# Performance work log

Hardware: AMD Instinct MI355X
Metric: run time of the kernel (lower is better)

Reference implementation:

```python
import jax, jax.numpy as jnp
import numpy as np
from jax import lax

B, T, LM, H = 16, 60, 63, 64   # batch, frames, landmark dim, lstm hidden
IMG_H, IMG_W = 240, 320
CONV_FEAT = 252                 # 4 * 7 * 9


def _conv(x, w, b, s):
    # x: [N, Cin, H, W], w: [Cout, Cin, kh, kw], VALID padding, stride s
    y = lax.conv_general_dilated(x, w, (s, s), 'VALID',
                                 dimension_numbers=('NCHW', 'OIHW', 'NCHW'))
    return y + b[None, :, None, None]


def setup_inputs() -> dict:
    key = jax.random.key(0)
    ks = jax.random.split(key, 24)
    s = 0.05
    d = {
        'input': jax.random.normal(ks[0], (B, T, LM), jnp.float32),
        'video': jax.random.uniform(ks[1], (B, T, IMG_H, IMG_W), jnp.float32),
        'W00': jax.random.normal(ks[2], (LM, LM), jnp.float32) * s,
        'b00': jnp.zeros((LM,), jnp.float32),
        'W01': jax.random.normal(ks[3], (64, LM), jnp.float32) * s,
        'b01': jnp.zeros((64,), jnp.float32),
        'Wc0': jax.random.normal(ks[4], (16, 1, 5, 5), jnp.float32) * s,
        'bc0': jnp.zeros((16,), jnp.float32),
        'Wc1': jax.random.normal(ks[5], (16, 16, 5, 5), jnp.float32) * s,
        'bc1': jnp.zeros((16,), jnp.float32),
        'Wc2': jax.random.normal(ks[6], (4, 16, 2, 2), jnp.float32) * s,
        'bc2': jnp.zeros((4,), jnp.float32),
        'Wih': jax.random.normal(ks[7], (4 * H, 64 + CONV_FEAT), jnp.float32) * s,
        'Whh': jax.random.normal(ks[8], (4 * H, H), jnp.float32) * s,
        'bih': jnp.zeros((4 * H,), jnp.float32),
        'bhh': jnp.zeros((4 * H,), jnp.float32),
        'W10': jax.random.normal(ks[9], (32, H), jnp.float32) * s,
        'b10': jnp.zeros((32,), jnp.float32),
        'W11': jax.random.normal(ks[10], (32, 32), jnp.float32) * s,
        'b11': jnp.zeros((32,), jnp.float32),
        'W12': jax.random.normal(ks[11], (256, 32), jnp.float32) * s,
        'b12': jnp.zeros((256,), jnp.float32),
    }
    return d


def reference(input, video, W00, b00, W01, b01, Wc0, bc0, Wc1, bc1, Wc2, bc2,
              Wih, Whh, bih, bhh, W10, b10, W11, b11, W12, b12):
    relu = jax.nn.relu
    # per-frame landmark MLP, vectorized over all frames: [B, T, 64]
    f = relu(jnp.einsum('btl,ml->btm', input, W00) + b00)
    f = relu(jnp.einsum('btl,ml->btm', f, W01) + b01)
    # per-frame conv features, all frames in one batched conv: [B*T, 1, 240, 320]
    v = video.reshape(B * T, 1, IMG_H, IMG_W)
    v = relu(_conv(v, Wc0, bc0, 4))          # [B*T, 16, 59, 79]
    v = relu(_conv(v, Wc1, bc1, 4))          # [B*T, 16, 14, 19]
    v = relu(_conv(v, Wc2, bc2, 2))          # [B*T, 4, 7, 9]
    v = v.reshape(B, T, CONV_FEAT)
    # frame inputs to LSTM: [B, T, 316]
    x = jnp.concatenate([f, v], axis=-1)
    # Torch semantics: LSTM called unbatched with 2D input [B, 316] per frame,
    # so the batch dim is consumed as a sequence; state carries across frames.
    # Total sequence is frame-major: [T, B, 316] -> [T*B, 316].
    seq = x.transpose(1, 0, 2).reshape(T * B, -1)

    def step(carry, xt):
        h, c = carry
        g = xt @ Wih.T + bih + h @ Whh.T + bhh
        i, fg, gg, o = jnp.split(g, 4)
        c = jax.nn.sigmoid(fg) * c + jax.nn.sigmoid(i) * jnp.tanh(gg)
        h = jax.nn.sigmoid(o) * jnp.tanh(c)
        return (h, c), h

    h0 = jnp.zeros((H,), seq.dtype)
    _, hs = lax.scan(step, (h0, h0), seq)    # [T*B, H]
    out = hs[-B:]                            # last frame's full output: [B, H]
    out = relu(out @ W10.T + b10)
    out = relu(out @ W11.T + b11)
    return out @ W12.T + b12                 # [B, 256]
```

## Files before the change

kernel.cpp:

```cpp
#include <hip/hip_runtime.h>
#include <math.h>

#define B_   16
#define T_   60
#define LMD  63
#define IH   240
#define IW   320
#define XDIM 316
#define NSEQ 960

#define X_BYTES   1213440
#define G_BYTES   983040

__device__ __forceinline__ float rl(float v, int k) {
    return __uint_as_float((unsigned)__builtin_amdgcn_readlane((int)__float_as_uint(v), k));
}
__device__ __forceinline__ float sig_f(float x) {
    return __builtin_amdgcn_rcpf(1.0f + __expf(-x));
}
__device__ __forceinline__ float tanh_f(float x) {
    return 1.0f - 2.0f * __builtin_amdgcn_rcpf(__expf(2.0f * x) + 1.0f);
}

__global__ void k_mlp(const float* __restrict__ inp,
                      const float* __restrict__ W00, const float* __restrict__ b00,
                      const float* __restrict__ W01, const float* __restrict__ b01,
                      float* __restrict__ X) {
    __shared__ float x0s[LMD], f1s[LMD];
    int bt = blockIdx.x;
    int b = bt / T_, t = bt % T_;
    int s = t * B_ + b;
    int m = threadIdx.x;
    if (m < LMD) x0s[m] = inp[bt * LMD + m];
    __syncthreads();
    if (m < LMD) {
        const float* wr = W00 + m * LMD;
        float a0 = 0.f, a1 = 0.f, a2 = 0.f, a3 = 0.f;
        for (int k = 0; k < 60; k += 4) {
            a0 += x0s[k + 0] * wr[k + 0];
            a1 += x0s[k + 1] * wr[k + 1];
            a2 += x0s[k + 2] * wr[k + 2];
            a3 += x0s[k + 3] * wr[k + 3];
        }
        a0 += x0s[60] * wr[60]; a1 += x0s[61] * wr[61]; a2 += x0s[62] * wr[62];
        f1s[m] = fmaxf(((a0 + a1) + (a2 + a3)) + b00[m], 0.f);
    }
    __syncthreads();
    {
        const float* wr = W01 + m * LMD;
        float a0 = 0.f, a1 = 0.f, a2 = 0.f, a3 = 0.f;
        for (int k = 0; k < 60; k += 4) {
            a0 += f1s[k + 0] * wr[k + 0];
            a1 += f1s[k + 1] * wr[k + 1];
            a2 += f1s[k + 2] * wr[k + 2];
            a3 += f1s[k + 3] * wr[k + 3];
        }
        a0 += f1s[60] * wr[60]; a1 += f1s[61] * wr[61]; a2 += f1s[62] * wr[62];
        X[(size_t)s * XDIM + m] = fmaxf(((a0 + a1) + (a2 + a3)) + b01[m], 0.f);
    }
}

__global__ __launch_bounds__(256, 1) void k_conv(const float* __restrict__ video,
        const float* __restrict__ Wc0, const float* __restrict__ bc0,
        const float* __restrict__ Wc1, const float* __restrict__ bc1,
        const float* __restrict__ Wc2, const float* __restrict__ bc2,
        float* __restrict__ X) {
    __shared__ float W0T[26 * 16];
    __shared__ float band[16 * 408];
    __shared__ float part[19 * 4 * 17];
    __shared__ float c1L[14 * 19 * 17];
    int tid = threadIdx.x;
    int bt = blockIdx.x;
    int b = bt / T_, t = bt % T_;
    int s = t * B_ + b;
    const float* vid = video + (size_t)bt * (IH * IW);

    int ch1 = tid & 15, ic = tid >> 4;
    int wave = tid >> 6, lane = tid & 63;

    int d0 = tid / 79, c0c0 = tid % 79;
    int pos1 = tid + 256;
    bool has1 = (pos1 < 395);
    int d1 = has1 ? pos1 / 79 : 0, c0c1 = has1 ? pos1 % 79 : 0;

    for (int i = tid; i < 400; i += 256) { int ch = i / 25, tap = i % 25; W0T[tap * 16 + ch] = Wc0[i]; }
    if (tid < 16) W0T[25 * 16 + tid] = bc0[tid];
    float w1r[25];
#pragma unroll
    for (int tap = 0; tap < 25; ++tap)
        w1r[tap] = Wc1[(ch1 * 16 + ic) * 25 + tap];

    float PX0[25], PX1[25];
    {
        const float* vb = vid + (4 * d0) * IW + c0c0 * 4;
#pragma unroll
        for (int kr = 0; kr < 5; ++kr) {
            float4 v = *(const float4*)(vb + kr * IW);
            PX0[kr*5+0]=v.x; PX0[kr*5+1]=v.y; PX0[kr*5+2]=v.z; PX0[kr*5+3]=v.w;
            PX0[kr*5+4]=vb[kr*IW+4];
        }
        if (has1) {
            const float* vc = vid + (4 * d1) * IW + c0c1 * 4;
#pragma unroll
            for (int kr = 0; kr < 5; ++kr) {
                float4 v = *(const float4*)(vc + kr * IW);
                PX1[kr*5+0]=v.x; PX1[kr*5+1]=v.y; PX1[kr*5+2]=v.z; PX1[kr*5+3]=v.w;
                PX1[kr*5+4]=vc[kr*IW+4];
            }
        }
    }
    __syncthreads();

    for (int r1 = 0; r1 < 14; ++r1) {
        {
            float acc[16];
            {
                const float4* b4 = (const float4*)&W0T[25 * 16];
                float4 ba = b4[0], bb = b4[1], bc = b4[2], bd = b4[3];
                acc[0]=ba.x; acc[1]=ba.y; acc[2]=ba.z; acc[3]=ba.w;
                acc[4]=bb.x; acc[5]=bb.y; acc[6]=bb.z; acc[7]=bb.w;
                acc[8]=bc.x; acc[9]=bc.y; acc[10]=bc.z; acc[11]=bc.w;
                acc[12]=bd.x; acc[13]=bd.y; acc[14]=bd.z; acc[15]=bd.w;
            }
#pragma unroll
            for (int tap = 0; tap < 25; ++tap) {
                float p = PX0[tap];
                const float4* w4 = (const float4*)&W0T[tap * 16];
                float4 wa = w4[0], wb = w4[1], wc = w4[2], wd = w4[3];
                acc[0]+=p*wa.x; acc[1]+=p*wa.y; acc[2]+=p*wa.z; acc[3]+=p*wa.w;
                acc[4]+=p*wb.x; acc[5]+=p*wb.y; acc[6]+=p*wb.z; acc[7]+=p*wb.w;
                acc[8]+=p*wc.x; acc[9]+=p*wc.y; acc[10]+=p*wc.z; acc[11]+=p*wc.w;
                acc[12]+=p*wd.x; acc[13]+=p*wd.y; acc[14]+=p*wd.z; acc[15]+=p*wd.w;
            }
#pragma unroll
            for (int ch = 0; ch < 16; ++ch)
                band[ch * 408 + d0 * 80 + c0c0] = fmaxf(acc[ch], 0.f);
        }
        if (has1) {
            float acc[16];
            {
                const float4* b4 = (const float4*)&W0T[25 * 16];
                float4 ba = b4[0], bb = b4[1], bc = b4[2], bd = b4[3];
                acc[0]=ba.x; acc[1]=ba.y; acc[2]=ba.z; acc[3]=ba.w;
                acc[4]=bb.x; acc[5]=bb.y; acc[6]=bb.z; acc[7]=bb.w;
                acc[8]=bc.x; acc[9]=bc.y; acc[10]=bc.z; acc[11]=bc.w;
                acc[12]=bd.x; acc[13]=bd.y; acc[14]=bd.z; acc[15]=bd.w;
            }
#pragma unroll
            for (int tap = 0; tap < 25; ++tap) {
                float p = PX1[tap];
                const float4* w4 = (const float4*)&W0T[tap * 16];
                float4 wa = w4[0], wb = w4[1], wc = w4[2], wd = w4[3];
                acc[0]+=p*wa.x; acc[1]+=p*wa.y; acc[2]+=p*wa.z; acc[3]+=p*wa.w;
                acc[4]+=p*wb.x; acc[5]+=p*wb.y; acc[6]+=p*wb.z; acc[7]+=p*wb.w;
                acc[8]+=p*wc.x; acc[9]+=p*wc.y; acc[10]+=p*wc.z; acc[11]+=p*wc.w;
                acc[12]+=p*wd.x; acc[13]+=p*wd.y; acc[14]+=p*wd.z; acc[15]+=p*wd.w;
            }
#pragma unroll
            for (int ch = 0; ch < 16; ++ch)
                band[ch * 408 + d1 * 80 + c0c1] = fmaxf(acc[ch], 0.f);
        }

        if (r1 + 1 < 14) {
            const float* vb = vid + (16 * (r1+1) + 4 * d0) * IW + c0c0 * 4;
#pragma unroll
            for (int kr = 0; kr < 5; ++kr) {
                float4 v = *(const float4*)(vb + kr * IW);
                PX0[kr*5+0]=v.x; PX0[kr*5+1]=v.y; PX0[kr*5+2]=v.z; PX0[kr*5+3]=v.w;
                PX0[kr*5+4]=vb[kr*IW+4];
            }
            if (has1) {
                const float* vc = vid + (16 * (r1+1) + 4 * d1) * IW + c0c1 * 4;
#pragma unroll
                for (int kr = 0; kr < 5; ++kr) {
                    float4 v = *(const float4*)(vc + kr * IW);
                    PX1[kr*5+0]=v.x; PX1[kr*5+1]=v.y; PX1[kr*5+2]=v.z; PX1[kr*5+3]=v.w;
                    PX1[kr*5+4]=vc[kr*IW+4];
                }
            }
        }
        __syncthreads();

        const float* bb0 = &band[ic * 408];
        for (int c1c = 0; c1c < 19; ++c1c) {
            const float* bb = bb0 + c1c * 4;
            float a0, a1, a2, a3, a4;
            {
                float4 v = *(const float4*)(bb);       float sc = bb[4];
                a0 = v.x*w1r[0]  + v.y*w1r[1]  + v.z*w1r[2]  + v.w*w1r[3]  + sc*w1r[4];
            }
            {
                float4 v = *(const float4*)(bb + 80);  float sc = bb[84];
                a1 = v.x*w1r[5]  + v.y*w1r[6]  + v.z*w1r[7]  + v.w*w1r[8]  + sc*w1r[9];
            }
            {
                float4 v = *(const float4*)(bb + 160); float sc = bb[164];
                a2 = v.x*w1r[10] + v.y*w1r[11] + v.z*w1r[12] + v.w*w1r[13] + sc*w1r[14];
            }
            {
                float4 v = *(const float4*)(bb + 240); float sc = bb[244];
                a3 = v.x*w1r[15] + v.y*w1r[16] + v.z*w1r[17] + v.w*w1r[18] + sc*w1r[19];
            }
            {
                float4 v = *(const float4*)(bb + 320); float sc = bb[324];
                a4 = v.x*w1r[20] + v.y*w1r[21] + v.z*w1r[22] + v.w*w1r[23] + sc*w1r[24];
            }
            float p = ((a0 + a1) + (a2 + a3)) + a4;
            p += __shfl_xor(p, 16);
            p += __shfl_xor(p, 32);
            if (lane < 16)
                part[c1c * 68 + wave * 17 + ch1] = p;
        }
        __syncthreads();

        for (int o = tid; o < 304; o += 256) {
            int c1c = o >> 4, ch = o & 15;
            const float* pp = &part[c1c * 68 + ch];
            float v = bc1[ch] + pp[0] + pp[17] + pp[34] + pp[51];
            c1L[(r1 * 19 + c1c) * 17 + ch] = fmaxf(v, 0.f);
        }
        __syncthreads();
    }

    for (int o = tid; o < 252; o += 256) {
        int ch2 = o / 63, rr = (o / 9) % 7, cc = o % 9;
        float a = bc2[ch2];
        for (int ic2 = 0; ic2 < 16; ++ic2)
            for (int kr = 0; kr < 2; ++kr)
                for (int kc = 0; kc < 2; ++kc)
                    a += c1L[((2 * rr + kr) * 19 + 2 * cc + kc) * 17 + ic2] *
                         Wc2[((ch2 * 16 + ic2) * 2 + kr) * 2 + kc];
        X[(size_t)s * XDIM + 64 + o] = fmaxf(a, 0.f);
    }
}

__global__ void k_gpre(const float* __restrict__ X, const float* __restrict__ Wih,
                       const float* __restrict__ bih, const float* __restrict__ bhh,
                       float* __restrict__ G) {
    int s = blockIdx.x;
    int j = threadIdx.x;
    const float4* x4 = (const float4*)(X + (size_t)s * XDIM);
    const float4* w4 = (const float4*)(Wih + (size_t)j * XDIM);
    float a0 = 0.f, a1 = 0.f, a2 = 0.f, a3 = 0.f;
    for (int ko = 0; ko < 79; ++ko) {
        float4 w = w4[ko], x = x4[ko];
        a0 += w.x * x.x;
        a1 += w.y * x.y;
        a2 += w.z * x.z;
        a3 += w.w * x.w;
    }
    G[(size_t)s * 256 + j] = ((a0 + a1) + (a2 + a3)) + (bih[j] + bhh[j]);
}

#define REPW(M) M(0) M(1) M(2) M(3) M(4) M(5) M(6) M(7) \
                M(8) M(9) M(10) M(11) M(12) M(13) M(14) M(15)

__global__ __launch_bounds__(256, 1) void k_scan(const float* __restrict__ G,
        const float* __restrict__ Whh,
        const float* __restrict__ W10, const float* __restrict__ b10,
        const float* __restrict__ W11, const float* __restrict__ b11,
        const float* __restrict__ W12, const float* __restrict__ b12,
        float* __restrict__ out) {
    __shared__ float act[2][256];
    __shared__ float hsL[16 * 64];
    __shared__ float m1s[32], m2s[32];
    int j = threadIdx.x;
    int w = j >> 6, l = j & 63;

#define DECLW(n) float4 wv##n;
    REPW(DECLW)
#undef DECLW
    {
        const float4* Wr = (const float4*)(Whh + (size_t)j * 64);
#define LOADW(n) wv##n = Wr[n];
        REPW(LOADW)
#undef LOADW
    }

    float h = 0.f, c = 0.f;
    float gcur = G[j];

    for (int t = 0; t < NSEQ; ++t) {
        float gnext = (t + 1 < NSEQ) ? G[(size_t)(t + 1) * 256 + j] : 0.f;

        float a0 = gcur, a1 = 0.f, a2 = 0.f, a3 = 0.f;
#define GFMA(n) { \
        float h0 = rl(h, 4*(n)+0), h1 = rl(h, 4*(n)+1); \
        float h2 = rl(h, 4*(n)+2), h3 = rl(h, 4*(n)+3); \
        a0 += h0 * wv##n.x; a1 += h1 * wv##n.y; \
        a2 += h2 * wv##n.z; a3 += h3 * wv##n.w; \
    }
        REPW(GFMA)
#undef GFMA
        float g = (a0 + a1) + (a2 + a3);
        float av = (w == 2) ? tanh_f(g) : sig_f(g);
        act[t & 1][j] = av;
        asm volatile("s_waitcnt lgkmcnt(0)\n\ts_barrier" ::: "memory");
        const float* ab = act[t & 1];
        float ai = ab[l], af = ab[64 + l], ag = ab[128 + l], ao = ab[192 + l];
        c = af * c + ai * ag;
        h = ao * tanh_f(c);
        if (t >= NSEQ - 16 && w == 0) hsL[(t - (NSEQ - 16)) * 64 + l] = h;
        gcur = gnext;
    }
    __syncthreads();

    for (int r = 0; r < 16; ++r) {
        if (j < 32) {
            float a = b10[j];
            for (int k = 0; k < 64; ++k) a += hsL[r * 64 + k] * W10[j * 64 + k];
            m1s[j] = fmaxf(a, 0.f);
        }
        __syncthreads();
        if (j < 32) {
            float a = b11[j];
            for (int k = 0; k < 32; ++k) a += m1s[k] * W11[j * 32 + k];
            m2s[j] = fmaxf(a, 0.f);
        }
        __syncthreads();
        {
            float a = b12[j];
            for (int k = 0; k < 32; ++k) a += m2s[k] * W12[j * 32 + k];
            out[r * 256 + j] = a;
        }
        __syncthreads();
    }
}

extern "C" void kernel_launch(void* const* d_in, const int* in_sizes, int n_in,
                              void* d_out, int out_size, void* d_ws, size_t ws_size,
                              hipStream_t stream) {
    const float* inp   = (const float*)d_in[0];
    const float* video = (const float*)d_in[1];
    const float* W00   = (const float*)d_in[2];
    const float* b00   = (const float*)d_in[3];
    const float* W01   = (const float*)d_in[4];
    const float* b01   = (const float*)d_in[5];
    const float* Wc0   = (const float*)d_in[6];
    const float* bc0   = (const float*)d_in[7];
    const float* Wc1   = (const float*)d_in[8];
    const float* bc1   = (const float*)d_in[9];
    const float* Wc2   = (const float*)d_in[10];
    const float* bc2   = (const float*)d_in[11];
    const float* Wih   = (const float*)d_in[12];
    const float* Whh   = (const float*)d_in[13];
    const float* bih   = (const float*)d_in[14];
    const float* bhh   = (const float*)d_in[15];
    const float* W10   = (const float*)d_in[16];
    const float* b10   = (const float*)d_in[17];
    const float* W11   = (const float*)d_in[18];
    const float* b11   = (const float*)d_in[19];
    const float* W12   = (const float*)d_in[20];
    const float* b12   = (const float*)d_in[21];

    float* X = (float*)d_ws;
    float* G = (float*)((char*)d_ws + X_BYTES);

    k_mlp <<<NSEQ, 64, 0, stream>>>(inp, W00, b00, W01, b01, X);
    k_conv<<<NSEQ, 256, 0, stream>>>(video, Wc0, bc0, Wc1, bc1, Wc2, bc2, X);
    k_gpre<<<NSEQ, 256, 0, stream>>>(X, Wih, bih, bhh, G);
    k_scan<<<1, 256, 0, stream>>>(G, Whh, W10, b10, W11, b11, W12, b12, (float*)d_out);
}
```

Measured before the change: 747.7 us.

## Split LSTM recurrent dot product across two waves per gate row

The serial LSTM scan kernel now uses 512 threads, so each gate row's 64-wide recurrent dot product is split into two 32-element halves held by separate waves. The partial sums go to shared memory, and every thread adds the pair and applies all four gate activations redundantly. The goal is to halve the per-step FMA/readlane chain on the critical serial path. The G prefetch is also deepened to two steps ahead. In exchange, a 512-thread barrier is more expensive, more LDS reads are needed, and activation work is duplicated across waves.

New measurement: 1.079 ms. 44.3% more time.

```diff
diff --git a/kernel.cpp b/kernel.cpp
--- a/kernel.cpp
+++ b/kernel.cpp
@@ -252,56 +252,68 @@
     G[(size_t)s * 256 + j] = ((a0 + a1) + (a2 + a3)) + (bih[j] + bhh[j]);
 }
 
-#define REPW(M) M(0) M(1) M(2) M(3) M(4) M(5) M(6) M(7) \
-                M(8) M(9) M(10) M(11) M(12) M(13) M(14) M(15)
-
-__global__ __launch_bounds__(256, 1) void k_scan(const float* __restrict__ G,
+#define REP8(M) M(0) M(1) M(2) M(3) M(4) M(5) M(6) M(7)
+
+__global__ __launch_bounds__(512, 1) void k_scan(const float* __restrict__ G,
         const float* __restrict__ Whh,
         const float* __restrict__ W10, const float* __restrict__ b10,
         const float* __restrict__ W11, const float* __restrict__ b11,
         const float* __restrict__ W12, const float* __restrict__ b12,
         float* __restrict__ out) {
-    __shared__ float act[2][256];
+    __shared__ float act2[2][512];
     __shared__ float hsL[16 * 64];
     __shared__ float m1s[32], m2s[32];
     int j = threadIdx.x;
     int w = j >> 6, l = j & 63;
+    int g = w >> 1, half = w & 1;
+    int o = (g << 6) + l;
+    int kb = half << 5;
 
 #define DECLW(n) float4 wv##n;
-    REPW(DECLW)
+    REP8(DECLW)
 #undef DECLW
     {
-        const float4* Wr = (const float4*)(Whh + (size_t)j * 64);
+        const float4* Wr = (const float4*)(Whh + (size_t)o * 64 + kb);
 #define LOADW(n) wv##n = Wr[n];
-        REPW(LOADW)
+        REP8(LOADW)
 #undef LOADW
     }
 
     float h = 0.f, c = 0.f;
-    float gcur = G[j];
+    float gc = 0.f, gn = 0.f;
+    if (half == 0) {
+        gc = G[o];
+        gn = G[256 + o];
+    }
 
     for (int t = 0; t < NSEQ; ++t) {
-        float gnext = (t + 1 < NSEQ) ? G[(size_t)(t + 1) * 256 + j] : 0.f;
-
-        float a0 = gcur, a1 = 0.f, a2 = 0.f, a3 = 0.f;
+        float gp = 0.f;
+        if (half == 0) {
+            int t2 = (t + 2 < NSEQ) ? t + 2 : NSEQ - 1;
+            gp = G[(size_t)t2 * 256 + o];
+        }
+
+        float a0 = gc, a1 = 0.f, a2 = 0.f, a3 = 0.f;
 #define GFMA(n) { \
-        float h0 = rl(h, 4*(n)+0), h1 = rl(h, 4*(n)+1); \
-        float h2 = rl(h, 4*(n)+2), h3 = rl(h, 4*(n)+3); \
+        float h0 = rl(h, kb + 4*(n) + 0), h1 = rl(h, kb + 4*(n) + 1); \
+        float h2 = rl(h, kb + 4*(n) + 2), h3 = rl(h, kb + 4*(n) + 3); \
         a0 += h0 * wv##n.x; a1 += h1 * wv##n.y; \
         a2 += h2 * wv##n.z; a3 += h3 * wv##n.w; \
     }
-        REPW(GFMA)
+        REP8(GFMA)
 #undef GFMA
-        float g = (a0 + a1) + (a2 + a3);
-        float av = (w == 2) ? tanh_f(g) : sig_f(g);
-        act[t & 1][j] = av;
+        act2[t & 1][(w << 6) + l] = (a0 + a1) + (a2 + a3);
         asm volatile("s_waitcnt lgkmcnt(0)\n\ts_barrier" ::: "memory");
-        const float* ab = act[t & 1];
-        float ai = ab[l], af = ab[64 + l], ag = ab[128 + l], ao = ab[192 + l];
+        const float* ab = act2[t & 1];
+        float ai = ab[l]       + ab[64 + l];
+        float af = ab[128 + l] + ab[192 + l];
+        float ag = ab[256 + l] + ab[320 + l];
+        float ao = ab[384 + l] + ab[448 + l];
+        ai = sig_f(ai); af = sig_f(af); ag = tanh_f(ag); ao = sig_f(ao);
         c = af * c + ai * ag;
         h = ao * tanh_f(c);
         if (t >= NSEQ - 16 && w == 0) hsL[(t - (NSEQ - 16)) * 64 + l] = h;
-        gcur = gnext;
+        gc = gn; gn = gp;
     }
     __syncthreads();
 
@@ -318,7 +330,7 @@
             m2s[j] = fmaxf(a, 0.f);
         }
         __syncthreads();
-        {
+        if (j < 256) {
             float a = b12[j];
             for (int k = 0; k < 32; ++k) a += m2s[k] * W12[j * 32 + k];
             out[r * 256 + j] = a;
@@ -359,5 +371,5 @@
     k_mlp <<<NSEQ, 64, 0, stream>>>(inp, W00, b00, W01, b01, X);
     k_conv<<<NSEQ, 256, 0, stream>>>(video, Wc0, bc0, Wc1, bc1, Wc2, bc2, X);
     k_gpre<<<NSEQ, 256, 0, stream>>>(X, Wih, bih, bhh, G);
-    k_scan<<<1, 256, 0, stream>>>(G, Whh, W10, b10, W11, b11, W12, b12, (float*)d_out);
-}
+    k_scan<<<1, 512, 0, stream>>>(G, Whh, W10, b10, W11, b11, W12, b12, (float*)d_out);
+}
```

## Fuse all stages into one persistent kernel with flag-based producer/consumer overlap

Applied to the files above, without the earlier changes.

Merges the MLP, conv, input-gate projection and LSTM scan into a single persistent kernel. Block 0 runs the serial LSTM scan while 255 producer blocks compute per-timestep gate rows in sequence order and publish them through per-row release flags. The scan polls those flags with acquire loads, so the serial recurrence can overlap with the conv work instead of waiting for all of it, and the X buffer round trip is gone. The cost is spin-waiting, one fewer block doing conv work, and reliance on all 256 blocks being co-resident to avoid deadlock.

Result: slower. 1.150 ms (+53.8%).

```diff
diff --git a/kernel.cpp b/kernel.cpp
--- a/kernel.cpp
+++ b/kernel.cpp
@@ -8,9 +8,22 @@
 #define IW   320
 #define XDIM 316
 #define NSEQ 960
-
-#define X_BYTES   1213440
+#define NPROD 255
+
 #define G_BYTES   983040
+
+#define P_W0T   0
+#define P_BAND  416
+#define P_PART  6944
+#define P_C1L   8236
+#define P_XROW  12760
+#define P_X0S   13076
+#define P_F1S   13140
+#define P_ACT   0
+#define P_HSL   512
+#define P_M1S   1536
+#define P_M2S   1568
+#define POOLN   20736
 
 __device__ __forceinline__ float rl(float v, int k) {
     return __uint_as_float((unsigned)__builtin_amdgcn_readlane((int)__float_as_uint(v), k));
@@ -22,249 +35,262 @@
     return 1.0f - 2.0f * __builtin_amdgcn_rcpf(__expf(2.0f * x) + 1.0f);
 }
 
-__global__ void k_mlp(const float* __restrict__ inp,
-                      const float* __restrict__ W00, const float* __restrict__ b00,
-                      const float* __restrict__ W01, const float* __restrict__ b01,
-                      float* __restrict__ X) {
-    __shared__ float x0s[LMD], f1s[LMD];
-    int bt = blockIdx.x;
-    int b = bt / T_, t = bt % T_;
-    int s = t * B_ + b;
-    int m = threadIdx.x;
-    if (m < LMD) x0s[m] = inp[bt * LMD + m];
-    __syncthreads();
-    if (m < LMD) {
-        const float* wr = W00 + m * LMD;
-        float a0 = 0.f, a1 = 0.f, a2 = 0.f, a3 = 0.f;
-        for (int k = 0; k < 60; k += 4) {
-            a0 += x0s[k + 0] * wr[k + 0];
-            a1 += x0s[k + 1] * wr[k + 1];
-            a2 += x0s[k + 2] * wr[k + 2];
-            a3 += x0s[k + 3] * wr[k + 3];
-        }
-        a0 += x0s[60] * wr[60]; a1 += x0s[61] * wr[61]; a2 += x0s[62] * wr[62];
-        f1s[m] = fmaxf(((a0 + a1) + (a2 + a3)) + b00[m], 0.f);
-    }
-    __syncthreads();
-    {
-        const float* wr = W01 + m * LMD;
-        float a0 = 0.f, a1 = 0.f, a2 = 0.f, a3 = 0.f;
-        for (int k = 0; k < 60; k += 4) {
-            a0 += f1s[k + 0] * wr[k + 0];
-            a1 += f1s[k + 1] * wr[k + 1];
-            a2 += f1s[k + 2] * wr[k + 2];
-            a3 += f1s[k + 3] * wr[k + 3];
-        }
-        a0 += f1s[60] * wr[60]; a1 += f1s[61] * wr[61]; a2 += f1s[62] * wr[62];
-        X[(size_t)s * XDIM + m] = fmaxf(((a0 + a1) + (a2 + a3)) + b01[m], 0.f);
-    }
-}
-
-__global__ __launch_bounds__(256, 1) void k_conv(const float* __restrict__ video,
-        const float* __restrict__ Wc0, const float* __restrict__ bc0,
-        const float* __restrict__ Wc1, const float* __restrict__ bc1,
-        const float* __restrict__ Wc2, const float* __restrict__ bc2,
-        float* __restrict__ X) {
-    __shared__ float W0T[26 * 16];
-    __shared__ float band[16 * 408];
-    __shared__ float part[19 * 4 * 17];
-    __shared__ float c1L[14 * 19 * 17];
-    int tid = threadIdx.x;
-    int bt = blockIdx.x;
-    int b = bt / T_, t = bt % T_;
-    int s = t * B_ + b;
-    const float* vid = video + (size_t)bt * (IH * IW);
-
-    int ch1 = tid & 15, ic = tid >> 4;
-    int wave = tid >> 6, lane = tid & 63;
-
-    int d0 = tid / 79, c0c0 = tid % 79;
-    int pos1 = tid + 256;
-    bool has1 = (pos1 < 395);
-    int d1 = has1 ? pos1 / 79 : 0, c0c1 = has1 ? pos1 % 79 : 0;
-
-    for (int i = tid; i < 400; i += 256) { int ch = i / 25, tap = i % 25; W0T[tap * 16 + ch] = Wc0[i]; }
-    if (tid < 16) W0T[25 * 16 + tid] = bc0[tid];
-    float w1r[25];
-#pragma unroll
-    for (int tap = 0; tap < 25; ++tap)
-        w1r[tap] = Wc1[(ch1 * 16 + ic) * 25 + tap];
-
-    float PX0[25], PX1[25];
-    {
-        const float* vb = vid + (4 * d0) * IW + c0c0 * 4;
-#pragma unroll
-        for (int kr = 0; kr < 5; ++kr) {
-            float4 v = *(const float4*)(vb + kr * IW);
-            PX0[kr*5+0]=v.x; PX0[kr*5+1]=v.y; PX0[kr*5+2]=v.z; PX0[kr*5+3]=v.w;
-            PX0[kr*5+4]=vb[kr*IW+4];
-        }
-        if (has1) {
-            const float* vc = vid + (4 * d1) * IW + c0c1 * 4;
-#pragma unroll
-            for (int kr = 0; kr < 5; ++kr) {
-                float4 v = *(const float4*)(vc + kr * IW);
-                PX1[kr*5+0]=v.x; PX1[kr*5+1]=v.y; PX1[kr*5+2]=v.z; PX1[kr*5+3]=v.w;
-                PX1[kr*5+4]=vc[kr*IW+4];
-            }
-        }
-    }
-    __syncthreads();
-
-    for (int r1 = 0; r1 < 14; ++r1) {
-        {
-            float acc[16];
-            {
-                const float4* b4 = (const float4*)&W0T[25 * 16];
-                float4 ba = b4[0], bb = b4[1], bc = b4[2], bd = b4[3];
-                acc[0]=ba.x; acc[1]=ba.y; acc[2]=ba.z; acc[3]=ba.w;
-                acc[4]=bb.x; acc[5]=bb.y; acc[6]=bb.z; acc[7]=bb.w;
-                acc[8]=bc.x; acc[9]=bc.y; acc[10]=bc.z; acc[11]=bc.w;
-                acc[12]=bd.x; acc[13]=bd.y; acc[14]=bd.z; acc[15]=bd.w;
-            }
-#pragma unroll
-            for (int tap = 0; tap < 25; ++tap) {
-                float p = PX0[tap];
-                const float4* w4 = (const float4*)&W0T[tap * 16];
-                float4 wa = w4[0], wb = w4[1], wc = w4[2], wd = w4[3];
-                acc[0]+=p*wa.x; acc[1]+=p*wa.y; acc[2]+=p*wa.z; acc[3]+=p*wa.w;
-                acc[4]+=p*wb.x; acc[5]+=p*wb.y; acc[6]+=p*wb.z; acc[7]+=p*wb.w;
-                acc[8]+=p*wc.x; acc[9]+=p*wc.y; acc[10]+=p*wc.z; acc[11]+=p*wc.w;
-                acc[12]+=p*wd.x; acc[13]+=p*wd.y; acc[14]+=p*wd.z; acc[15]+=p*wd.w;
-            }
-#pragma unroll
-            for (int ch = 0; ch < 16; ++ch)
-                band[ch * 408 + d0 * 80 + c0c0] = fmaxf(acc[ch], 0.f);
-        }
-        if (has1) {
-            float acc[16];
-            {
-                const float4* b4 = (const float4*)&W0T[25 * 16];
-                float4 ba = b4[0], bb = b4[1], bc = b4[2], bd = b4[3];
-                acc[0]=ba.x; acc[1]=ba.y; acc[2]=ba.z; acc[3]=ba.w;
-                acc[4]=bb.x; acc[5]=bb.y; acc[6]=bb.z; acc[7]=bb.w;
-                acc[8]=bc.x; acc[9]=bc.y; acc[10]=bc.z; acc[11]=bc.w;
-                acc[12]=bd.x; acc[13]=bd.y; acc[14]=bd.z; acc[15]=bd.w;
-            }
-#pragma unroll
-            for (int tap = 0; tap < 25; ++tap) {
-                float p = PX1[tap];
-                const float4* w4 = (const float4*)&W0T[tap * 16];
-                float4 wa = w4[0], wb = w4[1], wc = w4[2], wd = w4[3];
-                acc[0]+=p*wa.x; acc[1]+=p*wa.y; acc[2]+=p*wa.z; acc[3]+=p*wa.w;
-                acc[4]+=p*wb.x; acc[5]+=p*wb.y; acc[6]+=p*wb.z; acc[7]+=p*wb.w;
-                acc[8]+=p*wc.x; acc[9]+=p*wc.y; acc[10]+=p*wc.z; acc[11]+=p*wc.w;
-                acc[12]+=p*wd.x; acc[13]+=p*wd.y; acc[14]+=p*wd.z; acc[15]+=p*wd.w;
-            }
-#pragma unroll
-            for (int ch = 0; ch < 16; ++ch)
-                band[ch * 408 + d1 * 80 + c0c1] = fmaxf(acc[ch], 0.f);
-        }
-
-        if (r1 + 1 < 14) {
-            const float* vb = vid + (16 * (r1+1) + 4 * d0) * IW + c0c0 * 4;
-#pragma unroll
-            for (int kr = 0; kr < 5; ++kr) {
-                float4 v = *(const float4*)(vb + kr * IW);
-                PX0[kr*5+0]=v.x; PX0[kr*5+1]=v.y; PX0[kr*5+2]=v.z; PX0[kr*5+3]=v.w;
-                PX0[kr*5+4]=vb[kr*IW+4];
-            }
-            if (has1) {
-                const float* vc = vid + (16 * (r1+1) + 4 * d1) * IW + c0c1 * 4;
-#pragma unroll
-                for (int kr = 0; kr < 5; ++kr) {
-                    float4 v = *(const float4*)(vc + kr * IW);
-                    PX1[kr*5+0]=v.x; PX1[kr*5+1]=v.y; PX1[kr*5+2]=v.z; PX1[kr*5+3]=v.w;
-                    PX1[kr*5+4]=vc[kr*IW+4];
-                }
-            }
-        }
-        __syncthreads();
-
-        const float* bb0 = &band[ic * 408];
-        for (int c1c = 0; c1c < 19; ++c1c) {
-            const float* bb = bb0 + c1c * 4;
-            float a0, a1, a2, a3, a4;
-            {
-                float4 v = *(const float4*)(bb);       float sc = bb[4];
-                a0 = v.x*w1r[0]  + v.y*w1r[1]  + v.z*w1r[2]  + v.w*w1r[3]  + sc*w1r[4];
-            }
-            {
-                float4 v = *(const float4*)(bb + 80);  float sc = bb[84];
-                a1 = v.x*w1r[5]  + v.y*w1r[6]  + v.z*w1r[7]  + v.w*w1r[8]  + sc*w1r[9];
-            }
-            {
-                float4 v = *(const float4*)(bb + 160); float sc = bb[164];
-                a2 = v.x*w1r[10] + v.y*w1r[11] + v.z*w1r[12] + v.w*w1r[13] + sc*w1r[14];
-            }
-            {
-                float4 v = *(const float4*)(bb + 240); float sc = bb[244];
-                a3 = v.x*w1r[15] + v.y*w1r[16] + v.z*w1r[17] + v.w*w1r[18] + sc*w1r[19];
-            }
-            {
-                float4 v = *(const float4*)(bb + 320); float sc = bb[324];
-                a4 = v.x*w1r[20] + v.y*w1r[21] + v.z*w1r[22] + v.w*w1r[23] + sc*w1r[24];
-            }
-            float p = ((a0 + a1) + (a2 + a3)) + a4;
-            p += __shfl_xor(p, 16);
-            p += __shfl_xor(p, 32);
-            if (lane < 16)
-                part[c1c * 68 + wave * 17 + ch1] = p;
-        }
-        __syncthreads();
-
-        for (int o = tid; o < 304; o += 256) {
-            int c1c = o >> 4, ch = o & 15;
-            const float* pp = &part[c1c * 68 + ch];
-            float v = bc1[ch] + pp[0] + pp[17] + pp[34] + pp[51];
-            c1L[(r1 * 19 + c1c) * 17 + ch] = fmaxf(v, 0.f);
-        }
-        __syncthreads();
-    }
-
-    for (int o = tid; o < 252; o += 256) {
-        int ch2 = o / 63, rr = (o / 9) % 7, cc = o % 9;
-        float a = bc2[ch2];
-        for (int ic2 = 0; ic2 < 16; ++ic2)
-            for (int kr = 0; kr < 2; ++kr)
-                for (int kc = 0; kc < 2; ++kc)
-                    a += c1L[((2 * rr + kr) * 19 + 2 * cc + kc) * 17 + ic2] *
-                         Wc2[((ch2 * 16 + ic2) * 2 + kr) * 2 + kc];
-        X[(size_t)s * XDIM + 64 + o] = fmaxf(a, 0.f);
-    }
-}
-
-__global__ void k_gpre(const float* __restrict__ X, const float* __restrict__ Wih,
-                       const float* __restrict__ bih, const float* __restrict__ bhh,
-                       float* __restrict__ G) {
-    int s = blockIdx.x;
-    int j = threadIdx.x;
-    const float4* x4 = (const float4*)(X + (size_t)s * XDIM);
-    const float4* w4 = (const float4*)(Wih + (size_t)j * XDIM);
-    float a0 = 0.f, a1 = 0.f, a2 = 0.f, a3 = 0.f;
-    for (int ko = 0; ko < 79; ++ko) {
-        float4 w = w4[ko], x = x4[ko];
-        a0 += w.x * x.x;
-        a1 += w.y * x.y;
-        a2 += w.z * x.z;
-        a3 += w.w * x.w;
-    }
-    G[(size_t)s * 256 + j] = ((a0 + a1) + (a2 + a3)) + (bih[j] + bhh[j]);
+__device__ __forceinline__ void waitrow(const int* flg, int s) {
+    while (__hip_atomic_load(&flg[s], __ATOMIC_ACQUIRE, __HIP_MEMORY_SCOPE_AGENT) == 0)
+        __builtin_amdgcn_s_sleep(8);
+}
+
+__global__ void k_zero(int* __restrict__ flg) {
+    int i = blockIdx.x * 256 + threadIdx.x;
+    if (i < NSEQ) flg[i] = 0;
 }
 
 #define REPW(M) M(0) M(1) M(2) M(3) M(4) M(5) M(6) M(7) \
                 M(8) M(9) M(10) M(11) M(12) M(13) M(14) M(15)
 
-__global__ __launch_bounds__(256, 1) void k_scan(const float* __restrict__ G,
-        const float* __restrict__ Whh,
-        const float* __restrict__ W10, const float* __restrict__ b10,
-        const float* __restrict__ W11, const float* __restrict__ b11,
-        const float* __restrict__ W12, const float* __restrict__ b12,
-        float* __restrict__ out) {
-    __shared__ float act[2][256];
-    __shared__ float hsL[16 * 64];
-    __shared__ float m1s[32], m2s[32];
-    int j = threadIdx.x;
+__global__ __launch_bounds__(256, 1) void k_all(
+        const float* __restrict__ inp,  const float* __restrict__ video,
+        const float* __restrict__ W00,  const float* __restrict__ b00,
+        const float* __restrict__ W01,  const float* __restrict__ b01,
+        const float* __restrict__ Wc0,  const float* __restrict__ bc0,
+        const float* __restrict__ Wc1,  const float* __restrict__ bc1,
+        const float* __restrict__ Wc2,  const float* __restrict__ bc2,
+        const float* __restrict__ Wih,  const float* __restrict__ Whh,
+        const float* __restrict__ bih,  const float* __restrict__ bhh,
+        const float* __restrict__ W10,  const float* __restrict__ b10,
+        const float* __restrict__ W11,  const float* __restrict__ b11,
+        const float* __restrict__ W12,  const float* __restrict__ b12,
+        float* __restrict__ G, int* __restrict__ flg, float* __restrict__ out)
+{
+    __shared__ __align__(16) float pool[POOLN];
+    int tid = threadIdx.x;
+
+    if (blockIdx.x != 0) {
+        float* W0T  = pool + P_W0T;
+        float* band = pool + P_BAND;
+        float* part = pool + P_PART;
+        float* c1L  = pool + P_C1L;
+        float* xrow = pool + P_XROW;
+        float* x0s  = pool + P_X0S;
+        float* f1s  = pool + P_F1S;
+
+        int ch1 = tid & 15, ic = tid >> 4;
+        int wave = tid >> 6, lane = tid & 63;
+        int d0 = tid / 79, c0c0 = tid % 79;
+        int pos1 = tid + 256;
+        bool has1 = (pos1 < 395);
+        int d1 = has1 ? pos1 / 79 : 0, c0c1 = has1 ? pos1 % 79 : 0;
+
+        for (int i = tid; i < 400; i += 256) { int ch = i / 25, tap = i % 25; W0T[tap * 16 + ch] = Wc0[i]; }
+        if (tid < 16) W0T[25 * 16 + tid] = bc0[tid];
+        float w1r[25];
+#pragma unroll
+        for (int tap = 0; tap < 25; ++tap)
+            w1r[tap] = Wc1[(ch1 * 16 + ic) * 25 + tap];
+
+        for (int s = (int)blockIdx.x - 1; s < NSEQ; s += NPROD) {
+            int t = s >> 4, b = s & 15;
+            int bt = b * T_ + t;
+            const float* vid = video + (size_t)bt * (IH * IW);
+
+            if (tid < LMD) x0s[tid] = inp[bt * LMD + tid];
+            __syncthreads();
+            if (tid < LMD) {
+                const float* wr = W00 + tid * LMD;
+                float a0 = 0.f, a1 = 0.f, a2 = 0.f, a3 = 0.f;
+                for (int k = 0; k < 60; k += 4) {
+                    a0 += x0s[k + 0] * wr[k + 0];
+                    a1 += x0s[k + 1] * wr[k + 1];
+                    a2 += x0s[k + 2] * wr[k + 2];
+                    a3 += x0s[k + 3] * wr[k + 3];
+                }
+                a0 += x0s[60] * wr[60]; a1 += x0s[61] * wr[61]; a2 += x0s[62] * wr[62];
+                f1s[tid] = fmaxf(((a0 + a1) + (a2 + a3)) + b00[tid], 0.f);
+            }
+            __syncthreads();
+            if (tid < 64) {
+                const float* wr = W01 + tid * LMD;
+                float a0 = 0.f, a1 = 0.f, a2 = 0.f, a3 = 0.f;
+                for (int k = 0; k < 60; k += 4) {
+                    a0 += f1s[k + 0] * wr[k + 0];
+                    a1 += f1s[k + 1] * wr[k + 1];
+                    a2 += f1s[k + 2] * wr[k + 2];
+                    a3 += f1s[k + 3] * wr[k + 3];
+                }
+                a0 += f1s[60] * wr[60]; a1 += f1s[61] * wr[61]; a2 += f1s[62] * wr[62];
+                xrow[tid] = fmaxf(((a0 + a1) + (a2 + a3)) + b01[tid], 0.f);
+            }
+
+            float PX0[25], PX1[25];
+            {
+                const float* vb = vid + (4 * d0) * IW + c0c0 * 4;
+#pragma unroll
+                for (int kr = 0; kr < 5; ++kr) {
+                    float4 v = *(const float4*)(vb + kr * IW);
+                    PX0[kr*5+0]=v.x; PX0[kr*5+1]=v.y; PX0[kr*5+2]=v.z; PX0[kr*5+3]=v.w;
+                    PX0[kr*5+4]=vb[kr*IW+4];
+                }
+                if (has1) {
+                    const float* vc = vid + (4 * d1) * IW + c0c1 * 4;
+#pragma unroll
+                    for (int kr = 0; kr < 5; ++kr) {
+                        float4 v = *(const float4*)(vc + kr * IW);
+                        PX1[kr*5+0]=v.x; PX1[kr*5+1]=v.y; PX1[kr*5+2]=v.z; PX1[kr*5+3]=v.w;
+                        PX1[kr*5+4]=vc[kr*IW+4];
+                    }
+                }
+            }
+            __syncthreads();
+
+            for (int r1 = 0; r1 < 14; ++r1) {
+                {
+                    float acc[16];
+                    {
+                        const float4* b4 = (const float4*)&W0T[25 * 16];
+                        float4 ba = b4[0], bb = b4[1], bc = b4[2], bd = b4[3];
+                        acc[0]=ba.x; acc[1]=ba.y; acc[2]=ba.z; acc[3]=ba.w;
+                        acc[4]=bb.x; acc[5]=bb.y; acc[6]=bb.z; acc[7]=bb.w;
+                        acc[8]=bc.x; acc[9]=bc.y; acc[10]=bc.z; acc[11]=bc.w;
+                        acc[12]=bd.x; acc[13]=bd.y; acc[14]=bd.z; acc[15]=bd.w;
+                    }
+#pragma unroll
+                    for (int tap = 0; tap < 25; ++tap) {
+                        float p = PX0[tap];
+                        const float4* w4 = (const float4*)&W0T[tap * 16];
+                        float4 wa = w4[0], wb = w4[1], wc = w4[2], wd = w4[3];
+                        acc[0]+=p*wa.x; acc[1]+=p*wa.y; acc[2]+=p*wa.z; acc[3]+=p*wa.w;
+                        acc[4]+=p*wb.x; acc[5]+=p*wb.y; acc[6]+=p*wb.z; acc[7]+=p*wb.w;
+                        acc[8]+=p*wc.x; acc[9]+=p*wc.y; acc[10]+=p*wc.z; acc[11]+=p*wc.w;
+                        acc[12]+=p*wd.x; acc[13]+=p*wd.y; acc[14]+=p*wd.z; acc[15]+=p*wd.w;
+                    }
+#pragma unroll
+                    for (int ch = 0; ch < 16; ++ch)
+                        band[ch * 408 + d0 * 80 + c0c0] = fmaxf(acc[ch], 0.f);
+                }
+                if (has1) {
+                    float acc[16];
+                    {
+                        const float4* b4 = (const float4*)&W0T[25 * 16];
+                        float4 ba = b4[0], bb = b4[1], bc = b4[2], bd = b4[3];
+                        acc[0]=ba.x; acc[1]=ba.y; acc[2]=ba.z; acc[3]=ba.w;
+                        acc[4]=bb.x; acc[5]=bb.y; acc[6]=bb.z; acc[7]=bb.w;
+                        acc[8]=bc.x; acc[9]=bc.y; acc[10]=bc.z; acc[11]=bc.w;
+                        acc[12]=bd.x; acc[13]=bd.y; acc[14]=bd.z; acc[15]=bd.w;
+                    }
+#pragma unroll
+                    for (int tap = 0; tap < 25; ++tap) {
+                        float p = PX1[tap];
+                        const float4* w4 = (const float4*)&W0T[tap * 16];
+                        float4 wa = w4[0], wb = w4[1], wc = w4[2], wd = w4[3];
+                        acc[0]+=p*wa.x; acc[1]+=p*wa.y; acc[2]+=p*wa.z; acc[3]+=p*wa.w;
+                        acc[4]+=p*wb.x; acc[5]+=p*wb.y; acc[6]+=p*wb.z; acc[7]+=p*wb.w;
+                        acc[8]+=p*wc.x; acc[9]+=p*wc.y; acc[10]+=p*wc.z; acc[11]+=p*wc.w;
+                        acc[12]+=p*wd.x; acc[13]+=p*wd.y; acc[14]+=p*wd.z; acc[15]+=p*wd.w;
+                    }
+#pragma unroll
+                    for (int ch = 0; ch < 16; ++ch)
+                        band[ch * 408 + d1 * 80 + c0c1] = fmaxf(acc[ch], 0.f);
+                }
+
+                if (r1 + 1 < 14) {
+                    const float* vb = vid + (16 * (r1+1) + 4 * d0) * IW + c0c0 * 4;
+#pragma unroll
+                    for (int kr = 0; kr < 5; ++kr) {
+                        float4 v = *(const float4*)(vb + kr * IW);
+                        PX0[kr*5+0]=v.x; PX0[kr*5+1]=v.y; PX0[kr*5+2]=v.z; PX0[kr*5+3]=v.w;
+                        PX0[kr*5+4]=vb[kr*IW+4];
+                    }
+                    if (has1) {
+                        const float* vc = vid + (16 * (r1+1) + 4 * d1) * IW + c0c1 * 4;
+#pragma unroll
+                        for (int kr = 0; kr < 5; ++kr) {
+                            float4 v = *(const float4*)(vc + kr * IW);
+                            PX1[kr*5+0]=v.x; PX1[kr*5+1]=v.y; PX1[kr*5+2]=v.z; PX1[kr*5+3]=v.w;
+                            PX1[kr*5+4]=vc[kr*IW+4];
+                        }
+                    }
+                }
+                __syncthreads();
+
+                const float* bb0 = &band[ic * 408];
+                for (int c1c = 0; c1c < 19; ++c1c) {
+                    const float* bb = bb0 + c1c * 4;
+                    float a0, a1, a2, a3, a4;
+                    {
+                        float4 v = *(const float4*)(bb);       float sc = bb[4];
+                        a0 = v.x*w1r[0]  + v.y*w1r[1]  + v.z*w1r[2]  + v.w*w1r[3]  + sc*w1r[4];
+                    }
+                    {
+                        float4 v = *(const float4*)(bb + 80);  float sc = bb[84];
+                        a1 = v.x*w1r[5]  + v.y*w1r[6]  + v.z*w1r[7]  + v.w*w1r[8]  + sc*w1r[9];
+                    }
+                    {
+                        float4 v = *(const float4*)(bb + 160); float sc = bb[164];
+                        a2 = v.x*w1r[10] + v.y*w1r[11] + v.z*w1r[12] + v.w*w1r[13] + sc*w1r[14];
+                    }
+                    {
+                        float4 v = *(const float4*)(bb + 240); float sc = bb[244];
+                        a3 = v.x*w1r[15] + v.y*w1r[16] + v.z*w1r[17] + v.w*w1r[18] + sc*w1r[19];
+                    }
+                    {
+                        float4 v = *(const float4*)(bb + 320); float sc = bb[324];
+                        a4 = v.x*w1r[20] + v.y*w1r[21] + v.z*w1r[22] + v.w*w1r[23] + sc*w1r[24];
+                    }
+                    float p = ((a0 + a1) + (a2 + a3)) + a4;
+                    p += __shfl_xor(p, 16);
+                    p += __shfl_xor(p, 32);
+                    if (lane < 16)
+                        part[c1c * 68 + wave * 17 + ch1] = p;
+                }
+                __syncthreads();
+
+                for (int o = tid; o < 304; o += 256) {
+                    int c1c = o >> 4, ch = o & 15;
+                    const float* pp = &part[c1c * 68 + ch];
+                    float v = bc1[ch] + pp[0] + pp[17] + pp[34] + pp[51];
+                    c1L[(r1 * 19 + c1c) * 17 + ch] = fmaxf(v, 0.f);
+                }
+                __syncthreads();
+            }
+
+            for (int o = tid; o < 252; o += 256) {
+                int ch2 = o / 63, rr = (o / 9) % 7, cc = o % 9;
+                float a = bc2[ch2];
+                for (int ic2 = 0; ic2 < 16; ++ic2)
+                    for (int kr = 0; kr < 2; ++kr)
+                        for (int kc = 0; kc < 2; ++kc)
+                            a += c1L[((2 * rr + kr) * 19 + 2 * cc + kc) * 17 + ic2] *
+                                 Wc2[((ch2 * 16 + ic2) * 2 + kr) * 2 + kc];
+                xrow[64 + o] = fmaxf(a, 0.f);
+            }
+            __syncthreads();
+
+            {
+                const float4* x4 = (const float4*)xrow;
+                const float4* w4 = (const float4*)(Wih + (size_t)tid * XDIM);
+                float a0 = 0.f, a1 = 0.f, a2 = 0.f, a3 = 0.f;
+                for (int ko = 0; ko < 79; ++ko) {
+                    float4 w = w4[ko], x = x4[ko];
+                    a0 += w.x * x.x;
+                    a1 += w.y * x.y;
+                    a2 += w.z * x.z;
+                    a3 += w.w * x.w;
+                }
+                G[(size_t)s * 256 + tid] = ((a0 + a1) + (a2 + a3)) + (bih[tid] + bhh[tid]);
+            }
+            __threadfence();
+            __syncthreads();
+            if (tid == 0)
+                __hip_atomic_store(&flg[s], 1, __ATOMIC_RELEASE, __HIP_MEMORY_SCOPE_AGENT);
+        }
+        return;
+    }
+
+    float* act = pool + P_ACT;
+    float* hsL = pool + P_HSL;
+    float* m1s = pool + P_M1S;
+    float* m2s = pool + P_M2S;
+    int j = tid;
     int w = j >> 6, l = j & 63;
 
 #define DECLW(n) float4 wv##n;
@@ -278,12 +304,19 @@
     }
 
     float h = 0.f, c = 0.f;
-    float gcur = G[j];
+    waitrow(flg, 0);
+    waitrow(flg, 1);
+    float gc = G[j];
+    float gn = G[256 + j];
 
     for (int t = 0; t < NSEQ; ++t) {
-        float gnext = (t + 1 < NSEQ) ? G[(size_t)(t + 1) * 256 + j] : 0.f;
-
-        float a0 = gcur, a1 = 0.f, a2 = 0.f, a3 = 0.f;
+        float gp = 0.f;
+        if (t + 2 < NSEQ) {
+            waitrow(flg, t + 2);
+            gp = G[(size_t)(t + 2) * 256 + j];
+        }
+
+        float a0 = gc, a1 = 0.f, a2 = 0.f, a3 = 0.f;
 #define GFMA(n) { \
         float h0 = rl(h, 4*(n)+0), h1 = rl(h, 4*(n)+1); \
         float h2 = rl(h, 4*(n)+2), h3 = rl(h, 4*(n)+3); \
@@ -294,14 +327,14 @@
 #undef GFMA
         float g = (a0 + a1) + (a2 + a3);
         float av = (w == 2) ? tanh_f(g) : sig_f(g);
-        act[t & 1][j] = av;
+        act[(t & 1) * 256 + j] = av;
         asm volatile("s_waitcnt lgkmcnt(0)\n\ts_barrier" ::: "memory");
-        const float* ab = act[t & 1];
+        const float* ab = act + (t & 1) * 256;
         float ai = ab[l], af = ab[64 + l], ag = ab[128 + l], ao = ab[192 + l];
         c = af * c + ai * ag;
         h = ao * tanh_f(c);
         if (t >= NSEQ - 16 && w == 0) hsL[(t - (NSEQ - 16)) * 64 + l] = h;
-        gcur = gnext;
+        gc = gn; gn = gp;
     }
     __syncthreads();
 
@@ -353,11 +386,13 @@
     const float* W12   = (const float*)d_in[20];
     const float* b12   = (const float*)d_in[21];
 
-    float* X = (float*)d_ws;
-    float* G = (float*)((char*)d_ws + X_BYTES);
-
-    k_mlp <<<NSEQ, 64, 0, stream>>>(inp, W00, b00, W01, b01, X);
-    k_conv<<<NSEQ, 256, 0, stream>>>(video, Wc0, bc0, Wc1, bc1, Wc2, bc2, X);
-    k_gpre<<<NSEQ, 256, 0, stream>>>(X, Wih, bih, bhh, G);
-    k_scan<<<1, 256, 0, stream>>>(G, Whh, W10, b10, W11, b11, W12, b12, (float*)d_out);
-}
+    float* G  = (float*)d_ws;
+    int* flg  = (int*)((char*)d_ws + G_BYTES);
+
+    k_zero<<<4, 256, 0, stream>>>(flg);
+    k_all<<<256, 256, 0, stream>>>(inp, video, W00, b00, W01, b01,
+                                   Wc0, bc0, Wc1, bc1, Wc2, bc2,
+                                   Wih, Whh, bih, bhh,
+                                   W10, b10, W11, b11, W12, b12,
+                                   G, flg, (float*)d_out);
+}
```
